# Kernel optimization log

Measured on AMD Instinct MI355X. Metric: run time of the kernel, lower is better.

## Reference

```python
import math
import jax, jax.numpy as jnp
import numpy as np

BATCH, LENGTH, D_MODEL, D_STATE = 8, 2048, 1024, 64
DT_MIN, DT_MAX = 1e-3, 1e-1


def setup_inputs() -> dict:
    key = jax.random.key(0)
    k1, k2, k3, k4 = jax.random.split(key, 4)
    x = jax.random.normal(k1, (BATCH, LENGTH, D_MODEL), dtype=jnp.float32)
    # dt_init == 'random': log_dt ~ U[log(dt_min), log(dt_max)], dt_scale = 1.0
    log_dt = jax.random.uniform(k2, (D_MODEL,), dtype=jnp.float32) * (
        math.log(DT_MAX) - math.log(DT_MIN)) + math.log(DT_MIN)
    scale = 1.0 / math.sqrt(D_STATE)
    B = jax.random.normal(k3, (D_MODEL, D_STATE), dtype=jnp.float32) * scale
    C = jax.random.normal(k4, (D_MODEL, D_STATE), dtype=jnp.float32) * scale
    D = jnp.ones((D_MODEL,), dtype=jnp.float32)
    return {"x": x, "log_dt": log_dt, "B": B, "C": C, "D": D}


def reference(x, log_dt, B, C, D):
    """S4DKernel.forward(x, mode='conv') -> y of shape [batch, length, d_model]."""
    d_model, d_state = B.shape
    length = x.shape[1]
    # A buffer: -0.5 * [1..d_state]
    A = -0.5 * jnp.arange(1, d_state + 1, dtype=jnp.float32)  # [N]
    # ZOH discretization
    dt = jnp.exp(log_dt)                       # [D]
    dtA = dt[:, None] * A[None, :]             # [D, N]
    A_bar = jnp.exp(dtA)                       # [D, N]
    B_bar = jnp.expm1(dtA) / A[None, :] * B    # [D, N]
    # Vandermonde kernel: K[d, k] = sum_n C[d,n] * B_bar[d,n] * A_bar[d,n]^k
    k_range = jnp.arange(length, dtype=jnp.float32)                 # [L]
    log_A_bar = jnp.log(jnp.clip(A_bar, 1e-10))                     # [D, N]
    powers = jnp.exp(log_A_bar[:, :, None] * k_range[None, None, :])  # [D, N, L]
    kernel = jnp.einsum('dn,dnk->dk', C * B_bar, powers)            # [D, L]
    # FFT convolution (linear conv via 2L-point FFT)
    x_t = jnp.swapaxes(x, 1, 2)                # [B, D, L]
    fft_size = 2 * length
    x_f = jnp.fft.rfft(x_t, n=fft_size)        # [B, D, L+1]
    k_f = jnp.fft.rfft(kernel, n=fft_size)     # [D, L+1]
    y = jnp.fft.irfft(x_f * k_f[None], n=fft_size)[..., :length]
    y = y + D[None, :, None] * x_t             # skip connection
    return jnp.swapaxes(y, 1, 2)               # [B, L, D]
```

## Files before the change

kernel.cpp:

```cpp
#include <hip/hip_runtime.h>
#include <math.h>


namespace {
constexpr int kBatch = 8;
constexpr int kLen   = 2048;
constexpr int kD     = 1024;
constexpr int kN     = 64;
constexpr int kT     = 64;
constexpr int kC     = kLen / kT;

constexpr long kUElems = (long)kBatch * kC * kN * kD;
constexpr long kAOff   = kUElems;
constexpr long kCbOff  = kAOff + (long)kN * kD;
constexpr long kAtOff  = kCbOff + (long)kN * kD;
}

__global__ void s4d_coef_kernel(const float* __restrict__ log_dt,
                                const float* __restrict__ Bm,
                                const float* __restrict__ Cm,
                                float* __restrict__ ws) {
  int tid = blockIdx.x * blockDim.x + threadIdx.x;
  int d = tid & (kD - 1);
  int n = tid >> 10;
  float dt  = expf(log_dt[d]);
  float An  = -0.5f * (float)(n + 1);
  float dtA = dt * An;
  float a   = expf(dtA);
  float bbar = (expm1f(dtA) / An) * Bm[d * kN + n];
  float cb   = Cm[d * kN + n] * bbar;
  float aT   = expf(dtA * (float)kT);
  ws[kAOff  + (long)n * kD + d] = a;
  ws[kCbOff + (long)n * kD + d] = cb;
  ws[kAtOff + (long)n * kD + d] = aT;
}

__global__ __launch_bounds__(256) void s4d_state_kernel(
    const float* __restrict__ x, float* __restrict__ ws) {
  int tid = blockIdx.x * blockDim.x + threadIdx.x;
  int d  = tid & (kD - 1);
  int bc = tid >> 10;
  int b  = bc >> 5;
  int c  = bc & (kC - 1);

  const float* xp = x + ((long)b * kLen + (long)c * kT) * kD + d;
  float xv[kT];
#pragma unroll
  for (int t = 0; t < kT; ++t) xv[t] = xp[(long)t * kD];

  const float* ap = ws + kAOff + d;
  float* up = ws + ((long)(b * kC + c) * kN) * kD + d;
#pragma unroll 4
  for (int n = 0; n < kN; ++n) {
    float a = ap[(long)n * kD];
    float h = 0.f;
#pragma unroll
    for (int t = 0; t < kT; ++t) h = fmaf(h, a, xv[t]);
    up[(long)n * kD] = h;
  }
}

__global__ void s4d_scan_kernel(float* __restrict__ ws) {
  int tid = blockIdx.x * blockDim.x + threadIdx.x;
  int d  = tid & (kD - 1);
  int bn = tid >> 10;
  int n  = bn & (kN - 1);
  int b  = bn >> 6;
  float aT = ws[kAtOff + (long)n * kD + d];
  float* up = ws + ((long)b * kC * kN + n) * kD + d;
  const long cstride = (long)kN * kD;
  float s = 0.f;
#pragma unroll 1
  for (int c = 0; c < kC; ++c) {
    float u = up[(long)c * cstride];
    up[(long)c * cstride] = s;
    s = fmaf(aT, s, u);
  }
}

__global__ __launch_bounds__(256, 2) void s4d_out_kernel(
    const float* __restrict__ x, const float* __restrict__ Dv,
    float* __restrict__ y, const float* __restrict__ ws) {
  int tid = blockIdx.x * blockDim.x + threadIdx.x;
  int d  = tid & (kD - 1);
  int bc = tid >> 10;
  int b  = bc >> 5;
  int c  = bc & (kC - 1);

  const float* xp = x + ((long)b * kLen + (long)c * kT) * kD + d;
  float xv[kT];
#pragma unroll
  for (int t = 0; t < kT; ++t) xv[t] = xp[(long)t * kD];

  float Dd = Dv[d];
  float acc[kT];
#pragma unroll
  for (int t = 0; t < kT; ++t) acc[t] = Dd * xv[t];

  const float* ap  = ws + kAOff + d;
  const float* cbp = ws + kCbOff + d;
  const float* sp  = ws + ((long)(b * kC + c) * kN) * kD + d;
#pragma unroll 2
  for (int n = 0; n < kN; ++n) {
    float a  = ap[(long)n * kD];
    float cb = cbp[(long)n * kD];
    float h  = sp[(long)n * kD];
#pragma unroll
    for (int t = 0; t < kT; ++t) {
      h = fmaf(h, a, xv[t]);
      acc[t] = fmaf(cb, h, acc[t]);
    }
  }

  float* yp = y + ((long)b * kLen + (long)c * kT) * kD + d;
#pragma unroll
  for (int t = 0; t < kT; ++t) yp[(long)t * kD] = acc[t];
}

extern "C" void kernel_launch(void* const* d_in, const int* in_sizes, int n_in,
                              void* d_out, int out_size, void* d_ws, size_t ws_size,
                              hipStream_t stream) {
  const float* x      = (const float*)d_in[0];
  const float* log_dt = (const float*)d_in[1];
  const float* Bm     = (const float*)d_in[2];
  const float* Cm     = (const float*)d_in[3];
  const float* Dv     = (const float*)d_in[4];
  float* y  = (float*)d_out;
  float* ws = (float*)d_ws;

  hipLaunchKernelGGL(s4d_coef_kernel, dim3((kN * kD) / 256), dim3(256), 0, stream,
                     log_dt, Bm, Cm, ws);
  hipLaunchKernelGGL(s4d_state_kernel, dim3((kBatch * kC * kD) / 256), dim3(256), 0, stream,
                     x, ws);
  hipLaunchKernelGGL(s4d_scan_kernel, dim3((kBatch * kN * kD) / 256), dim3(256), 0, stream,
                     ws);
  hipLaunchKernelGGL(s4d_out_kernel, dim3((kBatch * kC * kD) / 256), dim3(256), 0, stream,
                     x, Dv, y, ws);
}
```

Before: 236.9 us.

## Restructure chunk kernels to keep per-state registers and stream time sub-tiles

The state and output kernels now hold all 64 state values in registers and walk the 64-step chunk in sub-tiles of 16 timesteps, so only 16 x values and accumulators are live at once instead of 64. The A and C*B coefficients are interleaved into one float2 array so each state index needs a single vector load. The output kernel also drops its min-blocks launch bound. The aim is to lower register pressure and overlap loads with FMAs, at the cost of re-reading the coefficients once per sub-tile and possible register spills from the 64-element state array.

```diff
diff --git a/kernel.cpp b/kernel.cpp
--- a/kernel.cpp
+++ b/kernel.cpp
@@ -8,12 +8,12 @@
 constexpr int kD     = 1024;
 constexpr int kN     = 64;
 constexpr int kT     = 64;
+constexpr int kTT    = 16;
 constexpr int kC     = kLen / kT;
 
-constexpr long kUElems = (long)kBatch * kC * kN * kD;
-constexpr long kAOff   = kUElems;
-constexpr long kCbOff  = kAOff + (long)kN * kD;
-constexpr long kAtOff  = kCbOff + (long)kN * kD;
+constexpr long kUElems  = (long)kBatch * kC * kN * kD;
+constexpr long kAcbOff  = kUElems;
+constexpr long kAtOff   = kAcbOff + 2L * kN * kD;
 }
 
 __global__ void s4d_coef_kernel(const float* __restrict__ log_dt,
@@ -30,8 +30,8 @@
   float bbar = (expm1f(dtA) / An) * Bm[d * kN + n];
   float cb   = Cm[d * kN + n] * bbar;
   float aT   = expf(dtA * (float)kT);
-  ws[kAOff  + (long)n * kD + d] = a;
-  ws[kCbOff + (long)n * kD + d] = cb;
+  ws[kAcbOff + 2L * ((long)n * kD + d)]     = a;
+  ws[kAcbOff + 2L * ((long)n * kD + d) + 1] = cb;
   ws[kAtOff + (long)n * kD + d] = aT;
 }
 
@@ -44,20 +44,31 @@
   int c  = bc & (kC - 1);
 
   const float* xp = x + ((long)b * kLen + (long)c * kT) * kD + d;
-  float xv[kT];
+  const float* ap = ws + kAcbOff + 2L * d;
+
+  float h[kN];
 #pragma unroll
-  for (int t = 0; t < kT; ++t) xv[t] = xp[(long)t * kD];
+  for (int n = 0; n < kN; ++n) h[n] = 0.f;
 
-  const float* ap = ws + kAOff + d;
+#pragma unroll 1
+  for (int tt = 0; tt < kT / kTT; ++tt) {
+    float xv[kTT];
+#pragma unroll
+    for (int t = 0; t < kTT; ++t) xv[t] = xp[(long)(tt * kTT + t) * kD];
+#pragma unroll
+    for (int t = 0; t < kTT; ++t) asm volatile("" : "+v"(xv[t]));
+#pragma unroll
+    for (int n = 0; n < kN; ++n) {
+      float a = ap[2L * (long)n * kD];
+      float hn = h[n];
+#pragma unroll
+      for (int t = 0; t < kTT; ++t) hn = fmaf(hn, a, xv[t]);
+      h[n] = hn;
+    }
+  }
   float* up = ws + ((long)(b * kC + c) * kN) * kD + d;
-#pragma unroll 4
-  for (int n = 0; n < kN; ++n) {
-    float a = ap[(long)n * kD];
-    float h = 0.f;
 #pragma unroll
-    for (int t = 0; t < kT; ++t) h = fmaf(h, a, xv[t]);
-    up[(long)n * kD] = h;
-  }
+  for (int n = 0; n < kN; ++n) up[(long)n * kD] = h[n];
 }
 
 __global__ void s4d_scan_kernel(float* __restrict__ ws) {
@@ -78,7 +89,7 @@
   }
 }
 
-__global__ __launch_bounds__(256, 2) void s4d_out_kernel(
+__global__ __launch_bounds__(256) void s4d_out_kernel(
     const float* __restrict__ x, const float* __restrict__ Dv,
     float* __restrict__ y, const float* __restrict__ ws) {
   int tid = blockIdx.x * blockDim.x + threadIdx.x;
@@ -87,34 +98,41 @@
   int b  = bc >> 5;
   int c  = bc & (kC - 1);
 
-  const float* xp = x + ((long)b * kLen + (long)c * kT) * kD + d;
-  float xv[kT];
+  const float2* acb = (const float2*)(ws + kAcbOff);
+  const float*  sp  = ws + ((long)(b * kC + c) * kN) * kD + d;
+
+  float h[kN];
 #pragma unroll
-  for (int t = 0; t < kT; ++t) xv[t] = xp[(long)t * kD];
+  for (int n = 0; n < kN; ++n) h[n] = sp[(long)n * kD];
 
   float Dd = Dv[d];
-  float acc[kT];
+  const float* xp = x + ((long)b * kLen + (long)c * kT) * kD + d;
+  float*       yp = y + ((long)b * kLen + (long)c * kT) * kD + d;
+
+#pragma unroll 1
+  for (int tt = 0; tt < kT / kTT; ++tt) {
+    float xv[kTT];
 #pragma unroll
-  for (int t = 0; t < kT; ++t) acc[t] = Dd * xv[t];
-
-  const float* ap  = ws + kAOff + d;
-  const float* cbp = ws + kCbOff + d;
-  const float* sp  = ws + ((long)(b * kC + c) * kN) * kD + d;
-#pragma unroll 2
-  for (int n = 0; n < kN; ++n) {
-    float a  = ap[(long)n * kD];
-    float cb = cbp[(long)n * kD];
-    float h  = sp[(long)n * kD];
+    for (int t = 0; t < kTT; ++t) xv[t] = xp[(long)(tt * kTT + t) * kD];
 #pragma unroll
-    for (int t = 0; t < kT; ++t) {
-      h = fmaf(h, a, xv[t]);
-      acc[t] = fmaf(cb, h, acc[t]);
+    for (int t = 0; t < kTT; ++t) asm volatile("" : "+v"(xv[t]));
+    float acc[kTT];
+#pragma unroll
+    for (int t = 0; t < kTT; ++t) acc[t] = Dd * xv[t];
+#pragma unroll
+    for (int n = 0; n < kN; ++n) {
+      float2 ac = acb[(long)n * kD + d];
+      float hn = h[n];
+#pragma unroll
+      for (int t = 0; t < kTT; ++t) {
+        hn = fmaf(hn, ac.x, xv[t]);
+        acc[t] = fmaf(ac.y, hn, acc[t]);
+      }
+      h[n] = hn;
     }
+#pragma unroll
+    for (int t = 0; t < kTT; ++t) yp[(long)(tt * kTT + t) * kD] = acc[t];
   }
-
-  float* yp = y + ((long)b * kLen + (long)c * kT) * kD + d;
-#pragma unroll
-  for (int t = 0; t < kT; ++t) yp[(long)t * kD] = acc[t];
 }
 
 extern "C" void kernel_launch(void* const* d_in, const int* in_sizes, int n_in,
```

After: 332.6 us. 40.4% more time.
